# Optimization experiments

Hardware: AMD Instinct MI355X
Metric: run time of the kernel (lower is better)

Reference implementation:

```python
import jax, jax.numpy as jnp
import numpy as np

D_MODEL = 2048
NUM_HEADS = 16
D_K = D_MODEL // NUM_HEADS

def setup_inputs() -> dict:
    key = jax.random.key(0)
    ks = jax.random.split(key, 5)
    scale = 1.0 / np.sqrt(D_MODEL)
    x = jax.random.normal(ks[0], (4, 2048, D_MODEL), dtype=jnp.float32)
    wq = jax.random.normal(ks[1], (D_MODEL, D_MODEL), dtype=jnp.float32) * scale
    wk = jax.random.normal(ks[2], (D_MODEL, D_MODEL), dtype=jnp.float32) * scale
    wv = jax.random.normal(ks[3], (D_MODEL, D_MODEL), dtype=jnp.float32) * scale
    wo = jax.random.normal(ks[4], (D_MODEL, D_MODEL), dtype=jnp.float32) * scale
    return {"x": x, "wq": wq, "wk": wk, "wv": wv, "wo": wo}

def reference(x, wq, wk, wv, wo):
    # torch Linear (no bias): y = x @ W^T
    B, S, _ = x.shape
    def split_heads(t):
        return t.reshape(B, S, NUM_HEADS, D_K).transpose(0, 2, 1, 3)  # [B,H,S,Dk]
    Q = split_heads(jnp.einsum('bsd,ed->bse', x, wq))
    K = split_heads(jnp.einsum('bsd,ed->bse', x, wk))
    V = split_heads(jnp.einsum('bsd,ed->bse', x, wv))
    scores = jnp.einsum('bhqd,bhkd->bhqk', Q, K) / jnp.sqrt(jnp.float32(D_K))
    attn = jax.nn.softmax(scores, axis=-1)  # dropout=0 (eval semantics)
    out = jnp.einsum('bhqk,bhkd->bhqd', attn, V)
    out = out.transpose(0, 2, 1, 3).reshape(B, S, D_MODEL)
    return jnp.einsum('bsd,ed->bse', out, wo)
```

## Files before the change

### kernel.cpp

```cpp
#include <hip/hip_runtime.h>
#include <math.h>

#define DMODEL 2048
#define NHEADS 16
#define DK     128
#define BATCH  4
#define SEQ    2048
#define MROWS  (BATCH*SEQ)

typedef unsigned short u16;
typedef short s16x8 __attribute__((ext_vector_type(8)));
typedef u16   u16x4 __attribute__((ext_vector_type(4)));
typedef u16   u16x8 __attribute__((ext_vector_type(8)));
typedef float f32x4 __attribute__((ext_vector_type(4)));
typedef unsigned int u32x2 __attribute__((ext_vector_type(2)));
typedef unsigned int u32x4 __attribute__((ext_vector_type(4)));

#define MFMA16(a, b, c) __builtin_amdgcn_mfma_f32_16x16x32_bf16((a), (b), (c), 0, 0, 0)

__device__ __forceinline__ u16 f2bf(float f) {
    unsigned u = __builtin_bit_cast(unsigned, f);
    unsigned r = (u + 0x7fffu + ((u >> 16) & 1u)) >> 16;
    return (u16)r;
}
__device__ __forceinline__ u16 f2bf_t(float f) {
    return (u16)(__builtin_bit_cast(unsigned, f) >> 16);
}
__device__ __forceinline__ float bf2f(u16 h) {
    unsigned u = ((unsigned)h) << 16;
    return __builtin_bit_cast(float, u);
}

__device__ __forceinline__ void gld_lds16(const u16* g, u16* l) {
    __builtin_amdgcn_global_load_lds(
        (const __attribute__((address_space(1))) unsigned int*)g,
        (__attribute__((address_space(3))) unsigned int*)l,
        16, 0, 0);
}

__global__ __launch_bounds__(256)
void split_bf16_kernel(const float* __restrict__ src,
                       u16* __restrict__ hi, u16* __restrict__ lo, int n8) {
    const int stride = gridDim.x * blockDim.x;
    for (int i = blockIdx.x * blockDim.x + threadIdx.x; i < n8; i += stride) {
        const float4 f0 = ((const float4*)src)[2 * i];
        const float4 f1 = ((const float4*)src)[2 * i + 1];
        const float f[8] = {f0.x, f0.y, f0.z, f0.w, f1.x, f1.y, f1.z, f1.w};
        u16x8 h8, l8;
#pragma unroll
        for (int j = 0; j < 8; ++j) {
            const u16 hb = f2bf_t(f[j]);
            h8[j] = hb;
            l8[j] = f2bf_t(f[j] - bf2f(hb));
        }
        ((u16x8*)hi)[i] = h8;
        ((u16x8*)lo)[i] = l8;
    }
}

__device__ __forceinline__ void gemm128_split_core(
        const u16* __restrict__ Ahg, const u16* __restrict__ Alg,
        const u16* __restrict__ Bhg, const u16* __restrict__ Blg,
        const int bm, const int bn, f32x4 (&acc)[4][4]) {
    __shared__ __align__(16) u16 Ah[128 * 32];
    __shared__ __align__(16) u16 Al[128 * 32];
    __shared__ __align__(16) u16 Bh[128 * 32];
    __shared__ __align__(16) u16 Bl[128 * 32];

    const int t    = threadIdx.x;
    const int lane = t & 63;
    const int wave = t >> 6;

    const int srow = t >> 2;
    const int skof = (t & 3) * 8;
    const size_t ga0 = (size_t)(bm + srow) * DMODEL + skof;
    const size_t ga1 = (size_t)(bm + srow + 64) * DMODEL + skof;
    const size_t gb0 = (size_t)(bn + srow) * DMODEL + skof;
    const size_t gb1 = (size_t)(bn + srow + 64) * DMODEL + skof;
    const int l0 = srow * 32 + skof;
    const int l1 = l0 + 64 * 32;

    const int lm = lane & 15;
    const int lg = lane >> 4;
    const int wr = (wave >> 1) * 64;
    const int wc = (wave & 1) * 64;
    const int aoff = (wr + lm) * 32 + lg * 8;
    const int boff = (wc + lm) * 32 + lg * 8;

    for (int kt = 0; kt < DMODEL; kt += 32) {
        __syncthreads();
        gld_lds16(Ahg + ga0 + kt, &Ah[l0]);
        gld_lds16(Ahg + ga1 + kt, &Ah[l1]);
        gld_lds16(Alg + ga0 + kt, &Al[l0]);
        gld_lds16(Alg + ga1 + kt, &Al[l1]);
        gld_lds16(Bhg + gb0 + kt, &Bh[l0]);
        gld_lds16(Bhg + gb1 + kt, &Bh[l1]);
        gld_lds16(Blg + gb0 + kt, &Bl[l0]);
        gld_lds16(Blg + gb1 + kt, &Bl[l1]);
        __syncthreads();

        s16x8 af[4], alf[4];
#pragma unroll
        for (int i = 0; i < 4; ++i) {
            af[i]  = *(const s16x8*)&Ah[aoff + i * 16 * 32];
            alf[i] = *(const s16x8*)&Al[aoff + i * 16 * 32];
        }
#pragma unroll
        for (int j = 0; j < 4; ++j) {
            const s16x8 bf  = *(const s16x8*)&Bh[boff + j * 16 * 32];
            const s16x8 blf = *(const s16x8*)&Bl[boff + j * 16 * 32];
#pragma unroll
            for (int i = 0; i < 4; ++i) {
                acc[i][j] = MFMA16(af[i],  bf,  acc[i][j]);
                acc[i][j] = MFMA16(alf[i], bf,  acc[i][j]);
                acc[i][j] = MFMA16(af[i],  blf, acc[i][j]);
            }
        }
    }
}

__global__ __launch_bounds__(256)
void qkv_proj_mfma(const u16* __restrict__ Xhi, const u16* __restrict__ Xlo,
                   const u16* __restrict__ Wh,  const u16* __restrict__ Wl,
                   u16* __restrict__ Qhi, u16* __restrict__ Qlo,
                   u16* __restrict__ Khi, u16* __restrict__ Klo,
                   u16* __restrict__ Vt) {
    const int g  = blockIdx.x >> 4;
    const int nb = blockIdx.x & 15;
    const int bm = blockIdx.y * 128;
    const size_t WE = (size_t)DMODEL * DMODEL;

    f32x4 acc[4][4] = {};
    gemm128_split_core(Xhi, Xlo, Wh + g * WE, Wl + g * WE, bm, nb * 128, acc);

    const int lane = threadIdx.x & 63;
    const int wave = threadIdx.x >> 6;
    const int lm = lane & 15;
    const int lg = lane >> 4;
    const int wr = (wave >> 1) * 64;
    const int wc = (wave & 1) * 64;

    if (g < 2) {
        u16* hiP = (g == 0) ? Qhi : Khi;
        u16* loP = (g == 0) ? Qlo : Klo;
        const float sc = (g == 0) ? 0.08838834764831845f : 1.0f;
#pragma unroll
        for (int i = 0; i < 4; ++i) {
#pragma unroll
            for (int r = 0; r < 4; ++r) {
                const int s  = bm + wr + i * 16 + lg * 4 + r;
                const int bb = s >> 11;
                const size_t base =
                    ((size_t)(bb * NHEADS + nb) * SEQ + (s & 2047)) * DK + wc + lm;
#pragma unroll
                for (int j = 0; j < 4; ++j) {
                    const float y = acc[i][j][r] * sc;
                    const u16 hb = f2bf_t(y);
                    hiP[base + j * 16] = hb;
                    loP[base + j * 16] = f2bf_t(y - bf2f(hb));
                }
            }
        }
    } else {
#pragma unroll
        for (int i = 0; i < 4; ++i) {
            const int s0 = bm + wr + i * 16 + lg * 4;
            const int bb = s0 >> 11;
            const int ss = s0 & 2047;
            const size_t rowb = (size_t)(bb * NHEADS + nb) * DK;
#pragma unroll
            for (int j = 0; j < 4; ++j) {
                u16x4 v;
#pragma unroll
                for (int r = 0; r < 4; ++r) v[r] = f2bf(acc[i][j][r]);
                *(u16x4*)(Vt + (rowb + wc + j * 16 + lm) * SEQ + ss) = v;
            }
        }
    }
}

__global__ __launch_bounds__(256)
void out_proj_mfma(const u16* __restrict__ Ohi, const u16* __restrict__ Olo,
                   const u16* __restrict__ Woh, const u16* __restrict__ Wol,
                   float* __restrict__ out) {
    const int bn = blockIdx.x * 128;
    const int bm = blockIdx.y * 128;
    f32x4 acc[4][4] = {};
    gemm128_split_core(Ohi, Olo, Woh, Wol, bm, bn, acc);

    const int lane = threadIdx.x & 63;
    const int wave = threadIdx.x >> 6;
    const int lm = lane & 15;
    const int lg = lane >> 4;
    const int wr = (wave >> 1) * 64;
    const int wc = (wave & 1) * 64;
#pragma unroll
    for (int i = 0; i < 4; ++i) {
#pragma unroll
        for (int r = 0; r < 4; ++r) {
            const int row = bm + wr + i * 16 + lg * 4 + r;
            float* dst = out + (size_t)row * DMODEL + bn + wc + lm;
#pragma unroll
            for (int j = 0; j < 4; ++j) dst[j * 16] = acc[i][j][r];
        }
    }
}

__global__ __launch_bounds__(256, 4)
void attn_kernel(const u16* __restrict__ Qhi, const u16* __restrict__ Qlo,
                 const u16* __restrict__ KhiG, const u16* __restrict__ KloG,
                 const u16* __restrict__ VtG,
                 u16* __restrict__ Ohi, u16* __restrict__ Olo) {
    __shared__ __align__(16) u16 Khs[32][136];
    __shared__ __align__(16) u16 Kls[32][136];
    __shared__ __align__(16) u16 Vs[128][40];
    __shared__ __align__(16) unsigned int Pw[256][12];

    const int idlin = blockIdx.y * gridDim.x + blockIdx.x;
    const int swz   = (idlin & 7) * 256 + (idlin >> 3);
    const int bh    = swz >> 5;
    const int q0    = (swz & 31) * 64;

    const int t  = threadIdx.x;
    const int l  = t & 63;
    const int w  = t >> 6;
    const int lm = l & 15;
    const int lg = l >> 4;
    const int woff = w * 16;

    s16x8 qh[4], ql[4];
    {
        const size_t qrow = (size_t)bh * SEQ + q0 + woff + lm;
#pragma unroll
        for (int kb = 0; kb < 4; ++kb) {
            const size_t off = qrow * DK + kb * 32 + lg * 8;
            qh[kb] = *(const s16x8*)(Qhi + off);
            ql[kb] = *(const s16x8*)(Qlo + off);
        }
    }

    f32x4 o[8];
#pragma unroll
    for (int nt = 0; nt < 8; ++nt) o[nt] = (f32x4){0.f, 0.f, 0.f, 0.f};
    float mrun = -1e30f;
    float lsm  = 0.f;

    const int skey = t >> 3;
    const int sdb  = (t & 7) * 16;
    const int vdim = t >> 1;
    const int vkb  = (t & 1) * 16;
    const u16* Kh_base = KhiG + ((size_t)bh * SEQ + skey) * DK + sdb;
    const u16* Kl_base = KloG + ((size_t)bh * SEQ + skey) * DK + sdb;
    const u16* Vt_base = VtG + ((size_t)bh * DK + vdim) * SEQ + vkb;

    const int prowA = w * 64 + ((2 * lg) & 3) * 16 + lm;
    const int prowB = w * 64 + ((2 * lg + 1) & 3) * 16 + lm;
    const int pcol  = (lg < 2) ? 0 : 2;

    u16x8 pk0 = *(const u16x8*)(Kh_base);
    u16x8 pk1 = *(const u16x8*)(Kh_base + 8);
    u16x8 pl0 = *(const u16x8*)(Kl_base);
    u16x8 pl1 = *(const u16x8*)(Kl_base + 8);
    u16x8 pv0 = *(const u16x8*)(Vt_base);
    u16x8 pv1 = *(const u16x8*)(Vt_base + 8);

    for (int kt = 0; kt < SEQ; kt += 32) {
        const int ktn = (kt + 32 < SEQ) ? kt + 32 : 0;
        const u16* khn = Kh_base + (size_t)ktn * DK;
        const u16* kln = Kl_base + (size_t)ktn * DK;
        const u16* vpn = Vt_base + ktn;
        const u16x8 nk0 = *(const u16x8*)khn;
        const u16x8 nk1 = *(const u16x8*)(khn + 8);
        const u16x8 nl0 = *(const u16x8*)kln;
        const u16x8 nl1 = *(const u16x8*)(kln + 8);
        const u16x8 nv0 = *(const u16x8*)vpn;
        const u16x8 nv1 = *(const u16x8*)(vpn + 8);

        __syncthreads();
        *(u16x8*)&Khs[skey][sdb]     = pk0;
        *(u16x8*)&Khs[skey][sdb + 8] = pk1;
        *(u16x8*)&Kls[skey][sdb]     = pl0;
        *(u16x8*)&Kls[skey][sdb + 8] = pl1;
        *(u16x8*)&Vs[vdim][vkb]      = pv0;
        *(u16x8*)&Vs[vdim][vkb + 8]  = pv1;
        __syncthreads();

        f32x4 sacc[2];
#pragma unroll
        for (int nt = 0; nt < 2; ++nt) {
            f32x4 acc = (f32x4){0.f, 0.f, 0.f, 0.f};
#pragma unroll
            for (int kb = 0; kb < 4; ++kb) {
                const s16x8 kh_f = *(const s16x8*)&Khs[nt * 16 + lm][kb * 32 + lg * 8];
                const s16x8 kl_f = *(const s16x8*)&Kls[nt * 16 + lm][kb * 32 + lg * 8];
                acc = MFMA16(kh_f, qh[kb], acc);
                acc = MFMA16(kl_f, qh[kb], acc);
                acc = MFMA16(kh_f, ql[kb], acc);
            }
            sacc[nt] = acc;
        }

        float pmax = fmaxf(fmaxf(fmaxf(sacc[0][0], sacc[0][1]),
                                 fmaxf(sacc[0][2], sacc[0][3])),
                           fmaxf(fmaxf(sacc[1][0], sacc[1][1]),
                                 fmaxf(sacc[1][2], sacc[1][3])));
        pmax = fmaxf(pmax, __shfl_xor(pmax, 16));
        pmax = fmaxf(pmax, __shfl_xor(pmax, 32));
        if (__any(pmax - mrun > 8.f)) {
            const float mnew = fmaxf(mrun, pmax);
            const float corr = __expf(mrun - mnew);
            mrun = mnew;
            lsm *= corr;
            float c4[4];
#pragma unroll
            for (int r = 0; r < 4; ++r) c4[r] = __shfl(corr, lg * 4 + r);
#pragma unroll
            for (int nt = 0; nt < 8; ++nt) {
#pragma unroll
                for (int r = 0; r < 4; ++r) o[nt][r] *= c4[r];
            }
        }
        float p[8];
#pragma unroll
        for (int r = 0; r < 4; ++r) {
            p[r]     = __expf(sacc[0][r] - mrun);
            p[4 + r] = __expf(sacc[1][r] - mrun);
        }
        float ls = ((p[0] + p[1]) + (p[2] + p[3])) +
                   ((p[4] + p[5]) + (p[6] + p[7]));
        ls += __shfl_xor(ls, 16);
        ls += __shfl_xor(ls, 32);
        lsm += ls;

        u32x4 hw, lw;
#pragma unroll
        for (int i = 0; i < 4; ++i) {
            const u16 h0 = f2bf_t(p[2 * i]);
            const u16 h1 = f2bf_t(p[2 * i + 1]);
            hw[i] = (unsigned)h0 | ((unsigned)h1 << 16);
            const u16 e0 = f2bf_t(p[2 * i] - bf2f(h0));
            const u16 e1 = f2bf_t(p[2 * i + 1] - bf2f(h1));
            lw[i] = (unsigned)e0 | ((unsigned)e1 << 16);
        }
        *(u32x4*)&Pw[t][0] = hw;
        *(u32x4*)&Pw[t][4] = lw;
        const u32x2 hA = *(const u32x2*)&Pw[prowA][pcol];
        const u32x2 hB = *(const u32x2*)&Pw[prowB][pcol];
        const u32x2 lA = *(const u32x2*)&Pw[prowA][pcol + 4];
        const u32x2 lB = *(const u32x2*)&Pw[prowB][pcol + 4];
        const u32x4 phw = {hA[0], hA[1], hB[0], hB[1]};
        const u32x4 plw = {lA[0], lA[1], lB[0], lB[1]};
        const s16x8 pHf = __builtin_bit_cast(s16x8, phw);
        const s16x8 pLf = __builtin_bit_cast(s16x8, plw);

#pragma unroll
        for (int nt = 0; nt < 8; ++nt) {
            const s16x8 vf = *(const s16x8*)&Vs[nt * 16 + lm][lg * 8];
            o[nt] = MFMA16(pHf, vf, o[nt]);
            o[nt] = MFMA16(pLf, vf, o[nt]);
        }

        pk0 = nk0; pk1 = nk1; pl0 = nl0; pl1 = nl1; pv0 = nv0; pv1 = nv1;
    }

    const int bb = bh >> 4;
    const int hh = bh & 15;
    const float invl = 1.f / lsm;
    float inv[4];
#pragma unroll
    for (int r = 0; r < 4; ++r) inv[r] = __shfl(invl, lg * 4 + r);
#pragma unroll
    for (int nt = 0; nt < 8; ++nt) {
#pragma unroll
        for (int r = 0; r < 4; ++r) {
            const int qrow = q0 + woff + lg * 4 + r;
            const size_t idx =
                ((size_t)bb * SEQ + qrow) * DMODEL + hh * DK + nt * 16 + lm;
            const float y = o[nt][r] * inv[r];
            const u16 hb = f2bf_t(y);
            Ohi[idx] = hb;
            Olo[idx] = f2bf_t(y - bf2f(hb));
        }
    }
}

extern "C" void kernel_launch(void* const* d_in, const int* in_sizes, int n_in,
                              void* d_out, int out_size, void* d_ws, size_t ws_size,
                              hipStream_t stream) {
    const float* x  = (const float*)d_in[0];
    const float* wq = (const float*)d_in[1];
    const float* wk = (const float*)d_in[2];
    const float* wv = (const float*)d_in[3];
    const float* wo = (const float*)d_in[4];

    const size_t NE = (size_t)MROWS * DMODEL;
    const size_t WE = (size_t)DMODEL * DMODEL;

    u16* Qhi = (u16*)d_ws;
    u16* Qlo = Qhi + NE;
    u16* Khi = Qhi + 2 * NE;
    u16* Klo = Qhi + 3 * NE;
    u16* Vt  = Qhi + 4 * NE;
    u16* Wqkvh = Qhi + 5 * NE;
    u16* Wqkvl = Wqkvh + 3 * WE;
    u16* Ohi = Qhi + 5 * NE;
    u16* Olo = Ohi + NE;
    u16* Woh = Qhi;
    u16* Wol = Woh + WE;
    u16* Xhi = (u16*)d_out;
    u16* Xlo = Xhi + NE;

    dim3 blk(256);
    split_bf16_kernel<<<dim3(1024), blk, 0, stream>>>(x, Xhi, Xlo, (int)(NE / 8));
    split_bf16_kernel<<<dim3(512), blk, 0, stream>>>(wq, Wqkvh, Wqkvl, (int)(WE / 8));
    split_bf16_kernel<<<dim3(512), blk, 0, stream>>>(wk, Wqkvh + WE, Wqkvl + WE, (int)(WE / 8));
    split_bf16_kernel<<<dim3(512), blk, 0, stream>>>(wv, Wqkvh + 2 * WE, Wqkvl + 2 * WE, (int)(WE / 8));

    qkv_proj_mfma<<<dim3(48, 64), blk, 0, stream>>>(Xhi, Xlo, Wqkvh, Wqkvl,
                                                    Qhi, Qlo, Khi, Klo, Vt);
    attn_kernel<<<dim3(SEQ / 64, BATCH * NHEADS), blk, 0, stream>>>(
        Qhi, Qlo, Khi, Klo, Vt, Ohi, Olo);

    split_bf16_kernel<<<dim3(512), blk, 0, stream>>>(wo, Woh, Wol, (int)(WE / 8));
    out_proj_mfma<<<dim3(16, 64), blk, 0, stream>>>(Ohi, Olo, Woh, Wol, (float*)d_out);
}
```

Baseline: 1.357 ms.

## Double-buffer LDS tiles in split-bf16 GEMM core to overlap loads with MFMA

The shared-memory tiles for the hi/lo A and B operands are doubled. The next k-tile's global-to-LDS loads are issued before the MFMAs on the current tile run, which leaves one barrier per iteration instead of two. The goal is to hide global load latency behind matrix math in the projection GEMMs. In exchange, LDS use per block doubles to 64KB, which may cut how many blocks fit on each CU.

New measurement: 1.382 ms. About the same (+1.8%).

```diff
diff --git a/kernel.cpp b/kernel.cpp
--- a/kernel.cpp
+++ b/kernel.cpp
@@ -62,10 +62,10 @@
         const u16* __restrict__ Ahg, const u16* __restrict__ Alg,
         const u16* __restrict__ Bhg, const u16* __restrict__ Blg,
         const int bm, const int bn, f32x4 (&acc)[4][4]) {
-    __shared__ __align__(16) u16 Ah[128 * 32];
-    __shared__ __align__(16) u16 Al[128 * 32];
-    __shared__ __align__(16) u16 Bh[128 * 32];
-    __shared__ __align__(16) u16 Bl[128 * 32];
+    __shared__ __align__(16) u16 Ah[2][128 * 32];
+    __shared__ __align__(16) u16 Al[2][128 * 32];
+    __shared__ __align__(16) u16 Bh[2][128 * 32];
+    __shared__ __align__(16) u16 Bl[2][128 * 32];
 
     const int t    = threadIdx.x;
     const int lane = t & 63;
@@ -87,28 +87,34 @@
     const int aoff = (wr + lm) * 32 + lg * 8;
     const int boff = (wc + lm) * 32 + lg * 8;
 
+#define STAGE(B, KT)                                  \
+    do {                                              \
+        gld_lds16(Ahg + ga0 + (KT), &Ah[B][l0]);      \
+        gld_lds16(Ahg + ga1 + (KT), &Ah[B][l1]);      \
+        gld_lds16(Alg + ga0 + (KT), &Al[B][l0]);      \
+        gld_lds16(Alg + ga1 + (KT), &Al[B][l1]);      \
+        gld_lds16(Bhg + gb0 + (KT), &Bh[B][l0]);      \
+        gld_lds16(Bhg + gb1 + (KT), &Bh[B][l1]);      \
+        gld_lds16(Blg + gb0 + (KT), &Bl[B][l0]);      \
+        gld_lds16(Blg + gb1 + (KT), &Bl[B][l1]);      \
+    } while (0)
+
+    STAGE(0, 0);
+    int cur = 0;
     for (int kt = 0; kt < DMODEL; kt += 32) {
         __syncthreads();
-        gld_lds16(Ahg + ga0 + kt, &Ah[l0]);
-        gld_lds16(Ahg + ga1 + kt, &Ah[l1]);
-        gld_lds16(Alg + ga0 + kt, &Al[l0]);
-        gld_lds16(Alg + ga1 + kt, &Al[l1]);
-        gld_lds16(Bhg + gb0 + kt, &Bh[l0]);
-        gld_lds16(Bhg + gb1 + kt, &Bh[l1]);
-        gld_lds16(Blg + gb0 + kt, &Bl[l0]);
-        gld_lds16(Blg + gb1 + kt, &Bl[l1]);
-        __syncthreads();
+        if (kt + 32 < DMODEL) STAGE(cur ^ 1, kt + 32);
 
         s16x8 af[4], alf[4];
 #pragma unroll
         for (int i = 0; i < 4; ++i) {
-            af[i]  = *(const s16x8*)&Ah[aoff + i * 16 * 32];
-            alf[i] = *(const s16x8*)&Al[aoff + i * 16 * 32];
+            af[i]  = *(const s16x8*)&Ah[cur][aoff + i * 16 * 32];
+            alf[i] = *(const s16x8*)&Al[cur][aoff + i * 16 * 32];
         }
 #pragma unroll
         for (int j = 0; j < 4; ++j) {
-            const s16x8 bf  = *(const s16x8*)&Bh[boff + j * 16 * 32];
-            const s16x8 blf = *(const s16x8*)&Bl[boff + j * 16 * 32];
+            const s16x8 bf  = *(const s16x8*)&Bh[cur][boff + j * 16 * 32];
+            const s16x8 blf = *(const s16x8*)&Bl[cur][boff + j * 16 * 32];
 #pragma unroll
             for (int i = 0; i < 4; ++i) {
                 acc[i][j] = MFMA16(af[i],  bf,  acc[i][j]);
@@ -116,7 +122,9 @@
                 acc[i][j] = MFMA16(af[i],  blf, acc[i][j]);
             }
         }
-    }
+        cur ^= 1;
+    }
+#undef STAGE
 }
 
 __global__ __launch_bounds__(256)
```
